# Kernel optimization log

Measured on AMD Instinct MI355X. Metric: run time of the kernel, lower is better.

Reference implementation:

```python
import jax, jax.numpy as jnp
import numpy as np
from jax import lax

KH, KW, PAD = 3, 3, 1  # kernel_size and paddings from init_kwargs


def _sign_pm1(v):
    # tf.sign with zeros mapped to -1
    return jnp.where(v > 0, jnp.float32(1.0), jnp.float32(-1.0)).astype(v.dtype)


def setup_inputs() -> dict:
    key = jax.random.key(0)
    k1, k2, k3 = jax.random.split(key, 3)
    x = jax.random.normal(k1, (32, 56, 56, 256), dtype=jnp.float32)
    kernel = jax.random.normal(k2, (KH, KW, 256, 256), dtype=jnp.float32) * 0.05
    bias = jax.random.normal(k3, (256,), dtype=jnp.float32) * 0.01
    return {"x": x, "kernel": kernel, "bias": bias}


def reference(x, kernel, bias):
    # pad input spatially (NHWC)
    xp = jnp.pad(x, ((0, 0), (PAD, PAD), (PAD, PAD), (0, 0)))

    # binarize kernel: static batch dim known -> alpha = mean(|W|) over (kh, kw, cin)
    bin_k = _sign_pm1(kernel)
    alpha = jnp.mean(jnp.abs(kernel), axis=(0, 1, 2))  # (Cout,)

    # binarize input: batch dim dynamic in TF -> beta = mean(|x|) over channels, keepdims
    bin_x = _sign_pm1(xp)                               # (N, H+2P, W+2P, C)
    beta = jnp.mean(jnp.abs(xp), axis=3, keepdims=True)  # (N, H+2P, W+2P, 1)

    # K = avg_pool(beta, kernel window, stride 1, VALID)
    K = lax.reduce_window(beta, jnp.float32(0.0), lax.add,
                          (1, KH, KW, 1), (1, 1, 1, 1), 'VALID') / (KH * KW)
    Ka = K * alpha  # (N, H, W, Cout) via broadcast

    conv = lax.conv_general_dilated(
        bin_x, bin_k, window_strides=(1, 1), padding='VALID',
        dimension_numbers=('NHWC', 'HWIO', 'NHWC'))  # (N, H, W, Cout)

    return conv * Ka + bias
```

## Files before the change

kernel.cpp:

```cpp
#include <hip/hip_runtime.h>
#include <cstdint>
#include <cstddef>

#define N_ 32
#define H_ 56
#define W_ 56
#define C_ 256
#define HP 58
#define WP 58

typedef int v4i  __attribute__((ext_vector_type(4)));
typedef int v16i __attribute__((ext_vector_type(16)));

__global__ __launch_bounds__(256) void pack_w(const float* __restrict__ k,
                                              signed char* __restrict__ wi8,
                                              float* __restrict__ palpha) {
    int idx = blockIdx.x;
    int p = idx >> 2, q = idx & 3;
    int co = threadIdx.x;
    float s = 0.f;
    #pragma unroll
    for (int half = 0; half < 2; ++half) {
        int kc = q * 2 + half;
        unsigned wrd[8];
        #pragma unroll
        for (int e = 0; e < 8; ++e) {
            unsigned wv = 0;
            #pragma unroll
            for (int j = 0; j < 4; ++j) {
                float v = k[(size_t)(p * 256 + kc * 32 + e * 4 + j) * 256 + co];
                s += fabsf(v);
                wv |= ((v > 0.f) ? 0x01u : 0xFFu) << (8 * j);
            }
            wrd[e] = wv;
        }
        v4i lo = {(int)wrd[0], (int)wrd[1], (int)wrd[2], (int)wrd[3]};
        v4i hi = {(int)wrd[4], (int)wrd[5], (int)wrd[6], (int)wrd[7]};
        size_t base = ((size_t)(p * 8 + kc) * 256 + co) * 2;
        ((v4i*)wi8)[base]     = lo;
        ((v4i*)wi8)[base + 1] = hi;
    }
    palpha[idx * 256 + co] = s;
}

__device__ __forceinline__ void epilogue(const v16i& acc, int mb, int svar,
                                         const float* bS, float alpha, float bv,
                                         int co, size_t obase,
                                         float* __restrict__ out) {
    #pragma unroll
    for (int r = 0; r < 16; ++r) {
        int row = (r & 3) + 8 * (r >> 2) + 4 * svar;
        int m = mb + row;
        if (m < 112) {
            int hl = (m >= 56);
            int w = m - 56 * hl;
            float val = (float)acc[r] * (bS[m] * alpha) + bv;
            out[obase + ((size_t)hl * W_ + w) * C_ + co] = val;
        }
    }
}

__global__ __launch_bounds__(512, 4) void bconv(
        const float4* __restrict__ x4,
        const signed char* __restrict__ wi8, const float* __restrict__ palpha,
        const float* __restrict__ bias, float* __restrict__ out) {
    int bid = blockIdx.x;
    int bi = (bid & 7) * 112 + (bid >> 3);
    int n = bi / 28;
    int hb = (bi - n * 28) * 2;

    int tid = threadIdx.x;
    int lane = tid & 63, wid = tid >> 6;
    int wm = wid >> 2, wn = wid & 3;
    int l31 = lane & 31, svar = lane >> 5;

    __shared__ __align__(16) signed char xs[4 * WP * 256];
    __shared__ float brow[4 * WP];
    __shared__ float bS[112];

    {
        int sl4 = lane >> 2;
        int bo  = (lane & 3) << 2;
        for (int i = 0; i < 29; ++i) {
            int pp = wid + 8 * i;
            int r = pp / WP, xc = pp - r * WP;
            int ypad = hb + r;
            bool inb = (ypad >= 1 && ypad <= H_ && xc >= 1 && xc <= W_);
            float4 v = make_float4(0.f, 0.f, 0.f, 0.f);
            if (inb)
                v = x4[(((size_t)n * H_ + (ypad - 1)) * W_ + (xc - 1)) * 64 + lane];
            unsigned wb = ((v.x > 0.f) ? 0x01u : 0xFFu)
                        | (((v.y > 0.f) ? 0x01u : 0xFFu) << 8)
                        | (((v.z > 0.f) ? 0x01u : 0xFFu) << 16)
                        | (((v.w > 0.f) ? 0x01u : 0xFFu) << 24);
            *(unsigned*)&xs[pp * 256 + ((sl4 ^ (pp & 15)) << 4) + bo] = wb;
            float s = fabsf(v.x) + fabsf(v.y) + fabsf(v.z) + fabsf(v.w);
            #pragma unroll
            for (int m = 32; m >= 1; m >>= 1) s += __shfl_xor(s, m, 64);
            if (lane == 0) brow[pp] = s * (1.f / 256.f);
        }
    }
    __syncthreads();

    if (tid < 112) {
        int r = (tid >= 56);
        int w = tid - 56 * r;
        float s = 0.f;
        #pragma unroll
        for (int rr = 0; rr < 3; ++rr)
            #pragma unroll
            for (int d = 0; d < 3; ++d) s += brow[(r + rr) * WP + w + d];
        bS[tid] = s * (1.f / 9.f);
    }

    int m0 = wm * 64 + l31;
    int m1 = m0 + 32;
    int m1e = m1 < 112 ? m1 : 111;
    int hl0 = (m0 >= 56), hl1 = (m1e >= 56);
    int pb0 = hl0 * WP + (m0 - 56 * hl0);
    int pb1 = hl1 * WP + (m1e - 56 * hl1);

    int co0 = wn * 64 + l31, co1 = co0 + 32;
    int vb0 = (co0 * 2 + svar);

    v16i acc00 = {0,0,0,0,0,0,0,0,0,0,0,0,0,0,0,0};
    v16i acc01 = acc00, acc10 = acc00, acc11 = acc00;

    const v4i* xsv = (const v4i*)xs;
    uint64_t wbase = (uint64_t)(uintptr_t)wi8;
    unsigned voff = (unsigned)vb0 * 16;

    v4i Bc0, Bc1;
    asm volatile("global_load_dwordx4 %0, %2, %3\n\t"
                 "global_load_dwordx4 %1, %2, %3 offset:1024"
                 : "=&v"(Bc0), "=&v"(Bc1) : "v"(voff), "s"(wbase));
    voff += 8192;

    for (int tap = 0; tap < 9; ++tap) {
        int kh = (tap * 11) >> 5;
        int kw = tap - kh * 3;
        int p0 = pb0 + kh * WP + kw;
        int p1 = pb1 + kh * WP + kw;
        int a0 = p0 << 4, x0 = p0 & 15;
        int a1 = p1 << 4, x1 = p1 & 15;
        #pragma unroll
        for (int kc = 0; kc < 8; ++kc) {
            v4i Bn0, Bn1;
            asm volatile("global_load_dwordx4 %0, %2, %3\n\t"
                         "global_load_dwordx4 %1, %2, %3 offset:1024"
                         : "=&v"(Bn0), "=&v"(Bn1) : "v"(voff), "s"(wbase));
            voff += 8192;
            int sl = kc * 2 + svar;
            v4i A0 = xsv[a0 | (sl ^ x0)];
            v4i A1 = xsv[a1 | (sl ^ x1)];
            asm volatile("s_waitcnt vmcnt(2)" ::: "memory");
            __builtin_amdgcn_sched_barrier(0);
            acc00 = __builtin_amdgcn_mfma_i32_32x32x32_i8(A0, Bc0, acc00, 0, 0, 0);
            acc10 = __builtin_amdgcn_mfma_i32_32x32x32_i8(A1, Bc0, acc10, 0, 0, 0);
            acc01 = __builtin_amdgcn_mfma_i32_32x32x32_i8(A0, Bc1, acc01, 0, 0, 0);
            acc11 = __builtin_amdgcn_mfma_i32_32x32x32_i8(A1, Bc1, acc11, 0, 0, 0);
            Bc0 = Bn0; Bc1 = Bn1;
        }
    }

    asm volatile("s_waitcnt vmcnt(0)" ::: "memory");
    __builtin_amdgcn_sched_barrier(0);

    __syncthreads();

    float a0s = 0.f, a1s = 0.f;
    for (int i = 0; i < 36; ++i) {
        a0s += palpha[i * 256 + co0];
        a1s += palpha[i * 256 + co1];
    }
    a0s *= (1.f / 2304.f);
    a1s *= (1.f / 2304.f);
    float bv0 = bias[co0], bv1 = bias[co1];

    size_t obase = (size_t)(n * H_ + hb) * W_ * C_;
    epilogue(acc00, wm * 64,      svar, bS, a0s, bv0, co0, obase, out);
    epilogue(acc01, wm * 64,      svar, bS, a1s, bv1, co1, obase, out);
    epilogue(acc10, wm * 64 + 32, svar, bS, a0s, bv0, co0, obase, out);
    epilogue(acc11, wm * 64 + 32, svar, bS, a1s, bv1, co1, obase, out);
}

extern "C" void kernel_launch(void* const* d_in, const int* in_sizes, int n_in,
                              void* d_out, int out_size, void* d_ws, size_t ws_size,
                              hipStream_t stream) {
    const float* x    = (const float*)d_in[0];
    const float* k    = (const float*)d_in[1];
    const float* bias = (const float*)d_in[2];
    float* out = (float*)d_out;

    char* ws = (char*)d_ws;
    signed char* wi8    = (signed char*)(ws);
    float*       palpha = (float*)(ws + 589824);

    pack_w<<<36, 256, 0, stream>>>(k, wi8, palpha);
    bconv<<<896, 512, 0, stream>>>((const float4*)x, wi8, palpha, bias, out);
}
```

Before: 258.1 us.

## Deepen weight prefetch to three stages and software-pipeline LDS operand reads

Weight fragments for the int8 MFMA loop now use a 4-slot register ring with three loads in flight instead of a single next-step buffer. Input-tile reads from LDS are issued one k-step ahead through inline ds_read_b128, with the address for the next tap computed early. The combined s_waitcnt on vmcnt and lgkmcnt is set to match the new depth, and s_setprio raises wave priority around each MFMA group. This aims to hide global and LDS latency in the inner loop, at the cost of more VGPRs per thread and a few extra weight loads past the last iteration.

```diff
diff --git a/kernel.cpp b/kernel.cpp
--- a/kernel.cpp
+++ b/kernel.cpp
@@ -120,54 +120,75 @@
     int pb0 = hl0 * WP + (m0 - 56 * hl0);
     int pb1 = hl1 * WP + (m1e - 56 * hl1);
 
-    int co0 = wn * 64 + l31, co1 = co0 + 32;
-    int vb0 = (co0 * 2 + svar);
+    int co0 = wn * 64 + l31;
+    unsigned ldsb = (unsigned)(uintptr_t)&xs[0];
 
     v16i acc00 = {0,0,0,0,0,0,0,0,0,0,0,0,0,0,0,0};
     v16i acc01 = acc00, acc10 = acc00, acc11 = acc00;
 
-    const v4i* xsv = (const v4i*)xs;
     uint64_t wbase = (uint64_t)(uintptr_t)wi8;
-    unsigned voff = (unsigned)vb0 * 16;
-
-    v4i Bc0, Bc1;
-    asm volatile("global_load_dwordx4 %0, %2, %3\n\t"
-                 "global_load_dwordx4 %1, %2, %3 offset:1024"
-                 : "=&v"(Bc0), "=&v"(Bc1) : "v"(voff), "s"(wbase));
-    voff += 8192;
+    unsigned voff = (unsigned)(co0 * 2 + svar) * 16;
+
+    v4i Bq0[4], Bq1[4];
+    #pragma unroll
+    for (int s = 0; s < 3; ++s) {
+        asm volatile("global_load_dwordx4 %0, %2, %3\n\t"
+                     "global_load_dwordx4 %1, %2, %3 offset:1024"
+                     : "=&v"(Bq0[s]), "=&v"(Bq1[s]) : "v"(voff), "s"(wbase));
+        voff += 8192;
+    }
+
+    unsigned t0 = ldsb + ((unsigned)pb0 << 8); int x0 = pb0 & 15;
+    unsigned t1 = ldsb + ((unsigned)pb1 << 8); int x1 = pb1 & 15;
+    v4i Aq0[2], Aq1[2];
+    asm volatile("ds_read_b128 %0, %1" : "=&v"(Aq0[0]) : "v"(t0 + (unsigned)((svar ^ x0) << 4)));
+    asm volatile("ds_read_b128 %0, %1" : "=&v"(Aq1[0]) : "v"(t1 + (unsigned)((svar ^ x1) << 4)));
 
     for (int tap = 0; tap < 9; ++tap) {
-        int kh = (tap * 11) >> 5;
-        int kw = tap - kh * 3;
-        int p0 = pb0 + kh * WP + kw;
-        int p1 = pb1 + kh * WP + kw;
-        int a0 = p0 << 4, x0 = p0 & 15;
-        int a1 = p1 << 4, x1 = p1 & 15;
         #pragma unroll
         for (int kc = 0; kc < 8; ++kc) {
-            v4i Bn0, Bn1;
             asm volatile("global_load_dwordx4 %0, %2, %3\n\t"
                          "global_load_dwordx4 %1, %2, %3 offset:1024"
-                         : "=&v"(Bn0), "=&v"(Bn1) : "v"(voff), "s"(wbase));
+                         : "=&v"(Bq0[(kc + 3) & 3]), "=&v"(Bq1[(kc + 3) & 3])
+                         : "v"(voff), "s"(wbase));
             voff += 8192;
-            int sl = kc * 2 + svar;
-            v4i A0 = xsv[a0 | (sl ^ x0)];
-            v4i A1 = xsv[a1 | (sl ^ x1)];
-            asm volatile("s_waitcnt vmcnt(2)" ::: "memory");
+            if (kc < 7) {
+                int sl = (kc + 1) * 2 + svar;
+                asm volatile("ds_read_b128 %0, %1" : "=&v"(Aq0[(kc + 1) & 1])
+                             : "v"(t0 + (unsigned)((sl ^ x0) << 4)));
+                asm volatile("ds_read_b128 %0, %1" : "=&v"(Aq1[(kc + 1) & 1])
+                             : "v"(t1 + (unsigned)((sl ^ x1) << 4)));
+            } else {
+                int tn = (tap < 8) ? tap + 1 : 8;
+                int khn = (tn * 11) >> 5, kwn = tn - khn * 3;
+                int p0n = pb0 + khn * WP + kwn;
+                int p1n = pb1 + khn * WP + kwn;
+                unsigned t0n = ldsb + ((unsigned)p0n << 8);
+                unsigned t1n = ldsb + ((unsigned)p1n << 8);
+                asm volatile("ds_read_b128 %0, %1" : "=&v"(Aq0[0])
+                             : "v"(t0n + (unsigned)((svar ^ (p0n & 15)) << 4)));
+                asm volatile("ds_read_b128 %0, %1" : "=&v"(Aq1[0])
+                             : "v"(t1n + (unsigned)((svar ^ (p1n & 15)) << 4)));
+                t0 = t0n; x0 = p0n & 15;
+                t1 = t1n; x1 = p1n & 15;
+            }
+            asm volatile("s_waitcnt vmcnt(6) lgkmcnt(2)" ::: "memory");
             __builtin_amdgcn_sched_barrier(0);
-            acc00 = __builtin_amdgcn_mfma_i32_32x32x32_i8(A0, Bc0, acc00, 0, 0, 0);
-            acc10 = __builtin_amdgcn_mfma_i32_32x32x32_i8(A1, Bc0, acc10, 0, 0, 0);
-            acc01 = __builtin_amdgcn_mfma_i32_32x32x32_i8(A0, Bc1, acc01, 0, 0, 0);
-            acc11 = __builtin_amdgcn_mfma_i32_32x32x32_i8(A1, Bc1, acc11, 0, 0, 0);
-            Bc0 = Bn0; Bc1 = Bn1;
-        }
-    }
-
-    asm volatile("s_waitcnt vmcnt(0)" ::: "memory");
+            __builtin_amdgcn_s_setprio(1);
+            acc00 = __builtin_amdgcn_mfma_i32_32x32x32_i8(Aq0[kc & 1], Bq0[kc & 3], acc00, 0, 0, 0);
+            acc10 = __builtin_amdgcn_mfma_i32_32x32x32_i8(Aq1[kc & 1], Bq0[kc & 3], acc10, 0, 0, 0);
+            acc01 = __builtin_amdgcn_mfma_i32_32x32x32_i8(Aq0[kc & 1], Bq1[kc & 3], acc01, 0, 0, 0);
+            acc11 = __builtin_amdgcn_mfma_i32_32x32x32_i8(Aq1[kc & 1], Bq1[kc & 3], acc11, 0, 0, 0);
+            __builtin_amdgcn_s_setprio(0);
+        }
+    }
+
+    asm volatile("s_waitcnt vmcnt(0) lgkmcnt(0)" ::: "memory");
     __builtin_amdgcn_sched_barrier(0);
 
     __syncthreads();
 
+    int co1 = co0 + 32;
     float a0s = 0.f, a1s = 0.f;
     for (int i = 0; i < 36; ++i) {
         a0s += palpha[i * 256 + co0];
```

Result: no change. 259.3 us (+0.5%).
